# Kernel optimization log

Hardware: AMD Instinct MI355X
Metric: run time of the kernel (lower is better)

Reference implementation:

```python
import jax, jax.numpy as jnp
import numpy as np

EMBED_DIM = 1024
NUM_HEADS = 16
HEAD_DIM = EMBED_DIM // NUM_HEADS
# Source divides by scale = head_dim**-0.5, i.e. multiplies logits by sqrt(head_dim).
INV_SCALE = float(HEAD_DIM) ** 0.5


def setup_inputs() -> dict:
    key = jax.random.key(0)
    ks = jax.random.split(key, 9)
    E = EMBED_DIM
    s = 1.0 / np.sqrt(E)
    x = jax.random.normal(ks[0], (2, 2048, E), dtype=jnp.float32)
    Wq = jax.random.uniform(ks[1], (E, E), jnp.float32, -s, s)
    bq = jax.random.uniform(ks[2], (E,), jnp.float32, -s, s)
    Wk = jax.random.uniform(ks[3], (E, E), jnp.float32, -s, s)
    bk = jax.random.uniform(ks[4], (E,), jnp.float32, -s, s)
    Wv = jax.random.uniform(ks[5], (E, E), jnp.float32, -s, s)
    bv = jax.random.uniform(ks[6], (E,), jnp.float32, -s, s)
    Wo = jax.random.uniform(ks[7], (E, E), jnp.float32, -s, s)
    bo = jax.random.uniform(ks[8], (E,), jnp.float32, -s, s)
    return {"x": x, "Wq": Wq, "bq": bq, "Wk": Wk, "bk": bk,
            "Wv": Wv, "bv": bv, "Wo": Wo, "bo": bo}


def reference(x, Wq, bq, Wk, bk, Wv, bv, Wo, bo):
    B, N, C = x.shape
    H, D = NUM_HEADS, HEAD_DIM
    # nn.Linear: y = x @ W.T + b
    q = (x @ Wq.T + bq).reshape(B, N, H, D).transpose(0, 2, 1, 3)  # [B,H,N,D]
    k = (x @ Wk.T + bk).reshape(B, N, H, D).transpose(0, 2, 1, 3)
    v = (x @ Wv.T + bv).reshape(B, N, H, D).transpose(0, 2, 1, 3)
    # Faithful to source: logits = QK^T / (head_dim**-0.5) = QK^T * sqrt(head_dim)
    logits = jnp.einsum('bhnd,bhmd->bhnm', q, k) * INV_SCALE  # [B,H,N,N]
    attn = jax.nn.softmax(logits, axis=-1)
    h = jnp.einsum('bhnm,bhmd->bhnd', attn, v)  # [B,H,N,D]
    concat_h = h.transpose(0, 2, 1, 3).reshape(B, N, C)
    return concat_h @ Wo.T + bo
```

## Files before the change

### kernel.cpp

```cpp
#include <hip/hip_runtime.h>
#include <math.h>

#define B_ 2
#define N_ 2048
#define E_ 1024
#define H_ 16
#define D_ 64

typedef unsigned short US;
typedef _Float16 h16x8 __attribute__((ext_vector_type(8)));
typedef __fp16 fp16x2 __attribute__((ext_vector_type(2)));
typedef float f32x4 __attribute__((ext_vector_type(4)));
#define MFMA16F(a,b,c) __builtin_amdgcn_mfma_f32_16x16x32_f16(a,b,c,0,0,0)
#define SCL  11.5415603828f

union HU { _Float16 h; US u; };
__device__ __forceinline__ US f2h(float f){ HU x; x.h = (_Float16)f; return x.u; }
__device__ __forceinline__ unsigned pkrtz(float a, float b){
  union { fp16x2 h; unsigned u; } x;
  x.h = __builtin_amdgcn_cvt_pkrtz(a, b);
  return x.u;
}

union U8 { US u[8]; uint4 v; };
union U4 { US u[4]; uint2 v; };

__device__ __forceinline__ void glds16(const US* g, US* l){
  __builtin_amdgcn_global_load_lds(
    (const __attribute__((address_space(1))) unsigned int*)(const void*)g,
    (__attribute__((address_space(3))) unsigned int*)(void*)l, 16, 0, 0);
}

__global__ __launch_bounds__(256) void conv_x(const float* __restrict__ x, US* __restrict__ hi)
{
  int i = (blockIdx.x*256 + threadIdx.x)*8;
  float f[8];
  *(float4*)&f[0] = *(const float4*)&x[i];
  *(float4*)&f[4] = *(const float4*)&x[i+4];
  U8 h;
  #pragma unroll
  for (int j=0;j<8;++j) h.u[j] = f2h(f[j]);
  *(uint4*)&hi[i] = h.v;
}

__global__ __launch_bounds__(256) void conv_w(const float* __restrict__ w0, const float* __restrict__ w1,
                                              const float* __restrict__ w2, const float* __restrict__ w3,
                                              US* __restrict__ d0, US* __restrict__ d1,
                                              US* __restrict__ d2, US* __restrict__ d3)
{
  const float* s; US* d;
  switch (blockIdx.y) {
    case 0: s=w0; d=d0; break;
    case 1: s=w1; d=d1; break;
    case 2: s=w2; d=d2; break;
    default: s=w3; d=d3; break;
  }
  int i = (blockIdx.x*256 + threadIdx.x)*8;
  float f[8];
  *(float4*)&f[0] = *(const float4*)&s[i];
  *(float4*)&f[4] = *(const float4*)&s[i+4];
  U8 h;
  #pragma unroll
  for (int j=0;j<8;++j) h.u[j] = f2h(f[j]);
  *(uint4*)&d[i] = h.v;
}

template<int MODE>
__global__ __launch_bounds__(256,4) void gemm_glds(
    const US* __restrict__ A,
    const US* __restrict__ W0, const US* __restrict__ W1, const US* __restrict__ W2,
    const float* __restrict__ b0, const float* __restrict__ b1, const float* __restrict__ b2,
    void* o0, void* o1, void* o2)
{
  __shared__ __align__(16) US sA[128*32];
  __shared__ __align__(16) US sW[64*32];
  const int z = (MODE==0) ? blockIdx.z : 0;
  const US* W = (z==0)?W0:(z==1)?W1:W2;
  const float* bias = (z==0)?b0:(z==1)?b1:b2;
  void* out = (z==0)?o0:(z==1)?o1:o2;

  const int t = threadIdx.x;
  const int w = t>>6, lane = t&63;
  const int q = lane>>4, c = lane&15;
  const int gm0 = blockIdx.y*128, gn0 = blockIdx.x*64;
  const int r16 = lane>>2, seg = lane&3;

  f32x4 acc[2][4] = {};
  for (int kb = 0; kb < 1024; kb += 32) {
    glds16(&A[(size_t)(gm0 + w*32      + r16)*1024 + kb + seg*8], &sA[(w*32)*32]);
    glds16(&A[(size_t)(gm0 + w*32 + 16 + r16)*1024 + kb + seg*8], &sA[(w*32+16)*32]);
    glds16(&W[(size_t)(gn0 + w*16      + r16)*1024 + kb + seg*8], &sW[(w*16)*32]);
    __syncthreads();
    h16x8 af[2], wf[4];
    #pragma unroll
    for (int rt=0;rt<2;++rt) af[rt] = *(const h16x8*)&sA[(w*32+rt*16+c)*32 + q*8];
    #pragma unroll
    for (int ct=0;ct<4;++ct) wf[ct] = *(const h16x8*)&sW[(ct*16+c)*32 + q*8];
    #pragma unroll
    for (int rt=0;rt<2;++rt)
      #pragma unroll
      for (int ct=0;ct<4;++ct)
        acc[rt][ct] = MFMA16F(af[rt], wf[ct], acc[rt][ct]);
    __syncthreads();
  }
  #pragma unroll
  for (int rt=0;rt<2;++rt)
  #pragma unroll
  for (int ct=0;ct<4;++ct) {
    int col = gn0 + ct*16 + c;
    float bv = bias[col];
    int rowb = gm0 + w*32 + rt*16 + q*4;
    if (MODE==0 && z==2) {
      int b = rowb>>11, n = rowb & (N_-1);
      int hh = col>>6, d = col & 63;
      U4 pk;
      #pragma unroll
      for (int r=0;r<4;++r) pk.u[r] = f2h(acc[rt][ct][r] + bv);
      *(uint2*)&((US*)out)[((size_t)(b*H_+hh)*D_ + d)*N_ + n] = pk.v;
    } else {
      #pragma unroll
      for (int r=0;r<4;++r) {
        int row = rowb + r;
        float v = acc[rt][ct][r] + bv;
        if (MODE==1) {
          ((float*)out)[(size_t)row*1024 + col] = v;
        } else {
          if (z==0) v *= SCL;
          int b = row>>11, n = row & (N_-1), hh = col>>6, d = col & 63;
          ((US*)out)[((size_t)(b*H_+hh)*N_+n)*D_ + d] = f2h(v);
        }
      }
    }
  }
}

#define KSTR2 72
#define VSTR  136
__global__ __launch_bounds__(256,2) void attn(
    const US* __restrict__ Qf, const US* __restrict__ Kf, const US* __restrict__ Vt,
    US* __restrict__ Hout)
{
  __shared__ __align__(16) US sK [128*KSTR2];
  __shared__ __align__(16) US sVt[64*VSTR];
  __shared__ __align__(16) US sP [4][16*VSTR];
  const int t = threadIdx.x;
  const int w = t>>6, lane = t&63, q = lane>>4, c = lane&15;
  const int id = blockIdx.x;
  const int bh = ((id & 7) << 2) | ((id >> 3) & 3);
  const int n0 = (id >> 5) * 128;
  const US* Kp = Kf + (size_t)bh * (N_*D_);
  const US* Vp = Vt + (size_t)bh * (D_*N_);

  h16x8 qb[2][2];
  #pragma unroll
  for (int g=0; g<2; ++g){
    const size_t qoff = (size_t)bh*(N_*D_) + (size_t)(n0 + w*32 + g*16 + c)*D_;
    qb[g][0] = *(const h16x8*)&Qf[qoff + q*8];
    qb[g][1] = *(const h16x8*)&Qf[qoff + 32 + q*8];
  }

  float mi[2] = {-INFINITY, -INFINITY};
  float ls[2] = {0.f, 0.f};
  f32x4 o[2][4] = {};

  const int kr = t>>3, kc8 = (t&7)*8;
  const int vr = t>>4, vc8 = (t&15)*8;

  for (int mt=0; mt<16; ++mt) {
    const int m0 = mt*128;
    #pragma unroll
    for (int p=0;p<4;++p){
      int r = p*32 + kr;
      *(uint4*)&sK[r*KSTR2 + kc8] = *(const uint4*)&Kp[(size_t)(m0 + r)*D_ + kc8];
    }
    #pragma unroll
    for (int p=0;p<4;++p){
      int r = p*16 + vr;
      *(uint4*)&sVt[r*VSTR + vc8] = *(const uint4*)&Vp[(size_t)r*N_ + m0 + vc8];
    }
    __syncthreads();

    f32x4 s[2][8];
    #pragma unroll
    for (int f=0; f<8; ++f){
      h16x8 k0 = *(const h16x8*)&sK[(f*16+c)*KSTR2 + q*8];
      h16x8 k1 = *(const h16x8*)&sK[(f*16+c)*KSTR2 + 32 + q*8];
      #pragma unroll
      for (int g=0; g<2; ++g){
        f32x4 sv = {};
        sv = MFMA16F(k0, qb[g][0], sv);
        sv = MFMA16F(k1, qb[g][1], sv);
        s[g][f] = sv;
      }
    }

    h16x8 pa[2][4];
    #pragma unroll
    for (int g=0; g<2; ++g){
      f32x4 vm = s[g][0];
      #pragma unroll
      for (int f=1; f<8; ++f){
        vm[0]=fmaxf(vm[0],s[g][f][0]); vm[1]=fmaxf(vm[1],s[g][f][1]);
        vm[2]=fmaxf(vm[2],s[g][f][2]); vm[3]=fmaxf(vm[3],s[g][f][3]);
      }
      float v = fmaxf(fmaxf(vm[0],vm[1]), fmaxf(vm[2],vm[3]));
      v = fmaxf(v, __shfl_xor(v, 16));
      v = fmaxf(v, __shfl_xor(v, 32));
      float mnew = fmaxf(mi[g], v);
      if (!__all(v <= mi[g])) {
        float alpha = exp2f(mi[g]-mnew);
        ls[g] *= alpha;
        float ar[4];
        #pragma unroll
        for (int r=0; r<4; ++r) ar[r] = __shfl(alpha, q*4+r);
        #pragma unroll
        for (int dt=0; dt<4; ++dt){
          o[g][dt][0]*=ar[0]; o[g][dt][1]*=ar[1]; o[g][dt][2]*=ar[2]; o[g][dt][3]*=ar[3];
        }
      }
      mi[g] = mnew;
      float ps = 0.f;
      #pragma unroll
      for (int f=0; f<8; ++f){
        #pragma unroll
        for (int r=0; r<4; ++r){
          float p = exp2f(s[g][f][r]-mnew);
          s[g][f][r] = p;
          ps += p;
        }
      }
      ls[g] += ps;
      #pragma unroll
      for (int f=0; f<8; ++f){
        uint2 pk;
        pk.x = pkrtz(s[g][f][0], s[g][f][1]);
        pk.y = pkrtz(s[g][f][2], s[g][f][3]);
        *(uint2*)&sP[w][c*VSTR + f*16 + q*4] = pk;
      }
      #pragma unroll
      for (int kc=0; kc<4; ++kc)
        pa[g][kc] = *(const h16x8*)&sP[w][c*VSTR + kc*32 + q*8];
    }

    #pragma unroll
    for (int dt=0; dt<4; ++dt){
      h16x8 vf[4];
      #pragma unroll
      for (int kc=0; kc<4; ++kc)
        vf[kc] = *(const h16x8*)&sVt[(dt*16+c)*VSTR + kc*32 + q*8];
      #pragma unroll
      for (int g=0; g<2; ++g)
        #pragma unroll
        for (int kc=0; kc<4; ++kc)
          o[g][dt] = MFMA16F(pa[g][kc], vf[kc], o[g][dt]);
    }
    __syncthreads();
  }

  const int b = bh>>4, hh = bh&15;
  #pragma unroll
  for (int g=0; g<2; ++g){
    float v = ls[g];
    v += __shfl_xor(v, 16);
    v += __shfl_xor(v, 32);
    float inv = 1.0f / v;
    float ir[4];
    #pragma unroll
    for (int r=0; r<4; ++r) ir[r] = __shfl(inv, q*4+r);
    #pragma unroll
    for (int dt=0; dt<4; ++dt){
      #pragma unroll
      for (int r=0; r<4; ++r){
        int n = n0 + w*32 + g*16 + q*4 + r;
        int d = dt*16 + c;
        Hout[((size_t)(b*N_+n)*H_+hh)*D_ + d] = f2h(o[g][dt][r] * ir[r]);
      }
    }
  }
}

extern "C" void kernel_launch(void* const* d_in, const int* in_sizes, int n_in,
                              void* d_out, int out_size, void* d_ws, size_t ws_size,
                              hipStream_t stream)
{
  const float* x  = (const float*)d_in[0];
  const float* Wq = (const float*)d_in[1];
  const float* bq = (const float*)d_in[2];
  const float* Wk = (const float*)d_in[3];
  const float* bk = (const float*)d_in[4];
  const float* Wv = (const float*)d_in[5];
  const float* bv = (const float*)d_in[6];
  const float* Wo = (const float*)d_in[7];
  const float* bo = (const float*)d_in[8];
  US* ws  = (US*)d_ws;
  const size_t M1 = 1048576;
  US* xh  = ws;
  US* Wqf = ws + 4*M1;
  US* Wkf = ws + 5*M1;
  US* Wvf = ws + 6*M1;
  US* Wof = ws + 7*M1;
  US* Qf  = ws + 8*M1;
  US* Kf  = ws + 12*M1;
  US* Vtb = ws + 16*M1;
  US* Hf  = ws + 20*M1;

  conv_x<<<2048, 256, 0, stream>>>(x, xh);
  conv_w<<<dim3(512,4,1), 256, 0, stream>>>(Wq, Wk, Wv, Wo, Wqf, Wkf, Wvf, Wof);

  gemm_glds<0><<<dim3(16,32,3), 256, 0, stream>>>(xh, Wqf, Wkf, Wvf, bq, bk, bv, Qf, Kf, Vtb);
  attn<<<512, 256, 0, stream>>>(Qf, Kf, Vtb, Hf);
  gemm_glds<1><<<dim3(16,32,1), 256, 0, stream>>>(Hf, Wof, nullptr, nullptr, bo, nullptr, nullptr, d_out, nullptr, nullptr);
}
```

Measured before the change: 231.1 us.

## Merge conversion kernels, fuse QKV GEMM tiles, compute softmax row sums via MFMA

The two fp32-to-fp16 conversion kernels become one launch. The QKV projection now computes all three outputs in a single block that shares each A tile across Q, K and V weights, which cuts the A reloads and removes the z grid dimension; this raises register and LDS use, so it launches with bounds (256,2). In attention, the scalar row-sum accumulation, its shuffles and the rescale are replaced by an extra MFMA against a ones vector that accumulates the denominator. That denominator now comes from the fp16-rounded probabilities, and it adds MFMA work in exchange for fewer VALU ops.

```diff
diff --git a/kernel.cpp b/kernel.cpp
--- a/kernel.cpp
+++ b/kernel.cpp
@@ -31,31 +31,22 @@
     (__attribute__((address_space(3))) unsigned int*)(void*)l, 16, 0, 0);
 }
 
-__global__ __launch_bounds__(256) void conv_x(const float* __restrict__ x, US* __restrict__ hi)
-{
-  int i = (blockIdx.x*256 + threadIdx.x)*8;
-  float f[8];
-  *(float4*)&f[0] = *(const float4*)&x[i];
-  *(float4*)&f[4] = *(const float4*)&x[i+4];
-  U8 h;
-  #pragma unroll
-  for (int j=0;j<8;++j) h.u[j] = f2h(f[j]);
-  *(uint4*)&hi[i] = h.v;
-}
-
-__global__ __launch_bounds__(256) void conv_w(const float* __restrict__ w0, const float* __restrict__ w1,
-                                              const float* __restrict__ w2, const float* __restrict__ w3,
-                                              US* __restrict__ d0, US* __restrict__ d1,
-                                              US* __restrict__ d2, US* __restrict__ d3)
-{
-  const float* s; US* d;
-  switch (blockIdx.y) {
-    case 0: s=w0; d=d0; break;
-    case 1: s=w1; d=d1; break;
-    case 2: s=w2; d=d2; break;
-    default: s=w3; d=d3; break;
-  }
-  int i = (blockIdx.x*256 + threadIdx.x)*8;
+__global__ __launch_bounds__(256) void conv_all(
+    const float* __restrict__ x,
+    const float* __restrict__ w0, const float* __restrict__ w1,
+    const float* __restrict__ w2, const float* __restrict__ w3,
+    US* __restrict__ xh, US* __restrict__ Wall)
+{
+  const int id = blockIdx.x;
+  const float* s; US* d; size_t off;
+  if (id < 2048) { s = x; d = xh; off = (size_t)id*2048; }
+  else {
+    int j = id - 2048, wsel = j>>9;
+    off = (size_t)(j&511)*2048;
+    s = (wsel==0)?w0:(wsel==1)?w1:(wsel==2)?w2:w3;
+    d = Wall + (size_t)wsel*1048576;
+  }
+  size_t i = off + (size_t)threadIdx.x*8;
   float f[8];
   *(float4*)&f[0] = *(const float4*)&s[i];
   *(float4*)&f[4] = *(const float4*)&s[i+4];
@@ -65,72 +56,111 @@
   *(uint4*)&d[i] = h.v;
 }
 
-template<int MODE>
-__global__ __launch_bounds__(256,4) void gemm_glds(
-    const US* __restrict__ A,
-    const US* __restrict__ W0, const US* __restrict__ W1, const US* __restrict__ W2,
-    const float* __restrict__ b0, const float* __restrict__ b1, const float* __restrict__ b2,
-    void* o0, void* o1, void* o2)
+__global__ __launch_bounds__(256,2) void qkv_gemm(
+    const US* __restrict__ A, const US* __restrict__ Wall,
+    const float* __restrict__ bq, const float* __restrict__ bk, const float* __restrict__ bv,
+    US* __restrict__ Qf, US* __restrict__ Kf, US* __restrict__ Vtb)
 {
   __shared__ __align__(16) US sA[128*32];
-  __shared__ __align__(16) US sW[64*32];
-  const int z = (MODE==0) ? blockIdx.z : 0;
-  const US* W = (z==0)?W0:(z==1)?W1:W2;
-  const float* bias = (z==0)?b0:(z==1)?b1:b2;
-  void* out = (z==0)?o0:(z==1)?o1:o2;
-
+  __shared__ __align__(16) US sW[192*32];
   const int t = threadIdx.x;
   const int w = t>>6, lane = t&63;
   const int q = lane>>4, c = lane&15;
   const int gm0 = blockIdx.y*128, gn0 = blockIdx.x*64;
   const int r16 = lane>>2, seg = lane&3;
 
+  f32x4 acc[3][2][4] = {};
+  for (int kb = 0; kb < 1024; kb += 32) {
+    glds16(&A[(size_t)(gm0 + w*32      + r16)*1024 + kb + seg*8], &sA[(w*32)*32]);
+    glds16(&A[(size_t)(gm0 + w*32 + 16 + r16)*1024 + kb + seg*8], &sA[(w*32+16)*32]);
+    #pragma unroll
+    for (int p=0;p<3;++p){
+      int cw = w*3 + p;
+      int z = cw>>2, r0 = (cw&3)*16;
+      glds16(&Wall[(size_t)z*1048576 + (size_t)(gn0 + r0 + r16)*1024 + kb + seg*8],
+             &sW[(z*64 + r0)*32]);
+    }
+    __syncthreads();
+    h16x8 af0 = *(const h16x8*)&sA[(w*32+c)*32 + q*8];
+    h16x8 af1 = *(const h16x8*)&sA[(w*32+16+c)*32 + q*8];
+    #pragma unroll
+    for (int z=0; z<3; ++z)
+      #pragma unroll
+      for (int ct=0; ct<4; ++ct){
+        h16x8 wf = *(const h16x8*)&sW[(z*64+ct*16+c)*32 + q*8];
+        acc[z][0][ct] = MFMA16F(af0, wf, acc[z][0][ct]);
+        acc[z][1][ct] = MFMA16F(af1, wf, acc[z][1][ct]);
+      }
+    __syncthreads();
+  }
+  #pragma unroll
+  for (int z=0; z<3; ++z)
+  #pragma unroll
+  for (int rt=0; rt<2; ++rt)
+  #pragma unroll
+  for (int ct=0; ct<4; ++ct) {
+    int col = gn0 + ct*16 + c;
+    float bv_ = (z==0 ? bq : z==1 ? bk : bv)[col];
+    int rowb = gm0 + w*32 + rt*16 + q*4;
+    int hh = col>>6, d = col & 63;
+    if (z==2) {
+      int b = rowb>>11, n = rowb & (N_-1);
+      U4 pk;
+      #pragma unroll
+      for (int r=0;r<4;++r) pk.u[r] = f2h(acc[z][rt][ct][r] + bv_);
+      *(uint2*)&Vtb[((size_t)(b*H_+hh)*D_ + d)*N_ + n] = pk.v;
+    } else {
+      US* dst = (z==0) ? Qf : Kf;
+      #pragma unroll
+      for (int r=0;r<4;++r) {
+        int row = rowb + r;
+        float v = acc[z][rt][ct][r] + bv_;
+        if (z==0) v *= SCL;
+        int b = row>>11, n = row & (N_-1);
+        dst[((size_t)(b*H_+hh)*N_+n)*D_ + d] = f2h(v);
+      }
+    }
+  }
+}
+
+__global__ __launch_bounds__(256,4) void o_gemm(
+    const US* __restrict__ A, const US* __restrict__ W,
+    const float* __restrict__ bias, float* __restrict__ out)
+{
+  __shared__ __align__(16) US sA[128*32];
+  __shared__ __align__(16) US sW[64*32];
+  const int t = threadIdx.x;
+  const int w = t>>6, lane = t&63;
+  const int q = lane>>4, c = lane&15;
+  const int gm0 = blockIdx.y*128, gn0 = blockIdx.x*64;
+  const int r16 = lane>>2, seg = lane&3;
+
   f32x4 acc[2][4] = {};
   for (int kb = 0; kb < 1024; kb += 32) {
     glds16(&A[(size_t)(gm0 + w*32      + r16)*1024 + kb + seg*8], &sA[(w*32)*32]);
     glds16(&A[(size_t)(gm0 + w*32 + 16 + r16)*1024 + kb + seg*8], &sA[(w*32+16)*32]);
     glds16(&W[(size_t)(gn0 + w*16      + r16)*1024 + kb + seg*8], &sW[(w*16)*32]);
     __syncthreads();
-    h16x8 af[2], wf[4];
-    #pragma unroll
-    for (int rt=0;rt<2;++rt) af[rt] = *(const h16x8*)&sA[(w*32+rt*16+c)*32 + q*8];
-    #pragma unroll
-    for (int ct=0;ct<4;++ct) wf[ct] = *(const h16x8*)&sW[(ct*16+c)*32 + q*8];
-    #pragma unroll
-    for (int rt=0;rt<2;++rt)
-      #pragma unroll
-      for (int ct=0;ct<4;++ct)
-        acc[rt][ct] = MFMA16F(af[rt], wf[ct], acc[rt][ct]);
-    __syncthreads();
-  }
-  #pragma unroll
-  for (int rt=0;rt<2;++rt)
-  #pragma unroll
-  for (int ct=0;ct<4;++ct) {
+    h16x8 af0 = *(const h16x8*)&sA[(w*32+c)*32 + q*8];
+    h16x8 af1 = *(const h16x8*)&sA[(w*32+16+c)*32 + q*8];
+    #pragma unroll
+    for (int ct=0; ct<4; ++ct){
+      h16x8 wf = *(const h16x8*)&sW[(ct*16+c)*32 + q*8];
+      acc[0][ct] = MFMA16F(af0, wf, acc[0][ct]);
+      acc[1][ct] = MFMA16F(af1, wf, acc[1][ct]);
+    }
+    __syncthreads();
+  }
+  #pragma unroll
+  for (int rt=0; rt<2; ++rt)
+  #pragma unroll
+  for (int ct=0; ct<4; ++ct) {
     int col = gn0 + ct*16 + c;
-    float bv = bias[col];
+    float bv_ = bias[col];
     int rowb = gm0 + w*32 + rt*16 + q*4;
-    if (MODE==0 && z==2) {
-      int b = rowb>>11, n = rowb & (N_-1);
-      int hh = col>>6, d = col & 63;
-      U4 pk;
-      #pragma unroll
-      for (int r=0;r<4;++r) pk.u[r] = f2h(acc[rt][ct][r] + bv);
-      *(uint2*)&((US*)out)[((size_t)(b*H_+hh)*D_ + d)*N_ + n] = pk.v;
-    } else {
-      #pragma unroll
-      for (int r=0;r<4;++r) {
-        int row = rowb + r;
-        float v = acc[rt][ct][r] + bv;
-        if (MODE==1) {
-          ((float*)out)[(size_t)row*1024 + col] = v;
-        } else {
-          if (z==0) v *= SCL;
-          int b = row>>11, n = row & (N_-1), hh = col>>6, d = col & 63;
-          ((US*)out)[((size_t)(b*H_+hh)*N_+n)*D_ + d] = f2h(v);
-        }
-      }
-    }
+    #pragma unroll
+    for (int r=0;r<4;++r)
+      out[(size_t)(rowb+r)*1024 + col] = acc[rt][ct][r] + bv_;
   }
 }
 
@@ -158,10 +188,12 @@
     qb[g][0] = *(const h16x8*)&Qf[qoff + q*8];
     qb[g][1] = *(const h16x8*)&Qf[qoff + 32 + q*8];
   }
+  h16x8 vones;
+  #pragma unroll
+  for (int j=0;j<8;++j) vones[j] = (_Float16)1.0f;
 
   float mi[2] = {-INFINITY, -INFINITY};
-  float ls[2] = {0.f, 0.f};
-  f32x4 o[2][4] = {};
+  f32x4 o[2][5] = {};
 
   const int kr = t>>3, kc8 = (t&7)*8;
   const int vr = t>>4, vc8 = (t&15)*8;
@@ -209,32 +241,24 @@
       float mnew = fmaxf(mi[g], v);
       if (!__all(v <= mi[g])) {
         float alpha = exp2f(mi[g]-mnew);
-        ls[g] *= alpha;
         float ar[4];
         #pragma unroll
         for (int r=0; r<4; ++r) ar[r] = __shfl(alpha, q*4+r);
         #pragma unroll
-        for (int dt=0; dt<4; ++dt){
+        for (int dt=0; dt<5; ++dt){
           o[g][dt][0]*=ar[0]; o[g][dt][1]*=ar[1]; o[g][dt][2]*=ar[2]; o[g][dt][3]*=ar[3];
         }
       }
       mi[g] = mnew;
-      float ps = 0.f;
       #pragma unroll
       for (int f=0; f<8; ++f){
-        #pragma unroll
-        for (int r=0; r<4; ++r){
-          float p = exp2f(s[g][f][r]-mnew);
-          s[g][f][r] = p;
-          ps += p;
-        }
-      }
-      ls[g] += ps;
-      #pragma unroll
-      for (int f=0; f<8; ++f){
+        float p0 = exp2f(s[g][f][0]-mnew);
+        float p1 = exp2f(s[g][f][1]-mnew);
+        float p2 = exp2f(s[g][f][2]-mnew);
+        float p3 = exp2f(s[g][f][3]-mnew);
         uint2 pk;
-        pk.x = pkrtz(s[g][f][0], s[g][f][1]);
-        pk.y = pkrtz(s[g][f][2], s[g][f][3]);
+        pk.x = pkrtz(p0, p1);
+        pk.y = pkrtz(p2, p3);
         *(uint2*)&sP[w][c*VSTR + f*16 + q*4] = pk;
       }
       #pragma unroll
@@ -254,19 +278,20 @@
         for (int kc=0; kc<4; ++kc)
           o[g][dt] = MFMA16F(pa[g][kc], vf[kc], o[g][dt]);
     }
+    #pragma unroll
+    for (int g=0; g<2; ++g)
+      #pragma unroll
+      for (int kc=0; kc<4; ++kc)
+        o[g][4] = MFMA16F(pa[g][kc], vones, o[g][4]);
     __syncthreads();
   }
 
   const int b = bh>>4, hh = bh&15;
   #pragma unroll
   for (int g=0; g<2; ++g){
-    float v = ls[g];
-    v += __shfl_xor(v, 16);
-    v += __shfl_xor(v, 32);
-    float inv = 1.0f / v;
     float ir[4];
     #pragma unroll
-    for (int r=0; r<4; ++r) ir[r] = __shfl(inv, q*4+r);
+    for (int r=0; r<4; ++r) ir[r] = 1.0f / o[g][4][r];
     #pragma unroll
     for (int dt=0; dt<4; ++dt){
       #pragma unroll
@@ -294,20 +319,15 @@
   const float* bo = (const float*)d_in[8];
   US* ws  = (US*)d_ws;
   const size_t M1 = 1048576;
-  US* xh  = ws;
-  US* Wqf = ws + 4*M1;
-  US* Wkf = ws + 5*M1;
-  US* Wvf = ws + 6*M1;
-  US* Wof = ws + 7*M1;
-  US* Qf  = ws + 8*M1;
-  US* Kf  = ws + 12*M1;
-  US* Vtb = ws + 16*M1;
-  US* Hf  = ws + 20*M1;
-
-  conv_x<<<2048, 256, 0, stream>>>(x, xh);
-  conv_w<<<dim3(512,4,1), 256, 0, stream>>>(Wq, Wk, Wv, Wo, Wqf, Wkf, Wvf, Wof);
-
-  gemm_glds<0><<<dim3(16,32,3), 256, 0, stream>>>(xh, Wqf, Wkf, Wvf, bq, bk, bv, Qf, Kf, Vtb);
+  US* xh   = ws;
+  US* Wall = ws + 4*M1;
+  US* Qf   = ws + 8*M1;
+  US* Kf   = ws + 12*M1;
+  US* Vtb  = ws + 16*M1;
+  US* Hf   = ws + 20*M1;
+
+  conv_all<<<4096, 256, 0, stream>>>(x, Wq, Wk, Wv, Wo, xh, Wall);
+  qkv_gemm<<<dim3(16,32), 256, 0, stream>>>(xh, Wall, bq, bk, bv, Qf, Kf, Vtb);
   attn<<<512, 256, 0, stream>>>(Qf, Kf, Vtb, Hf);
-  gemm_glds<1><<<dim3(16,32,1), 256, 0, stream>>>(Hf, Wof, nullptr, nullptr, bo, nullptr, nullptr, d_out, nullptr, nullptr);
-}
+  o_gemm<<<dim3(16,32), 256, 0, stream>>>(Hf, Wall + 3*M1, bo, (float*)d_out);
+}
```

Result: faster. 213.9 us (-7.4%).
